# Kernel optimization log

Measured on AMD Instinct MI355X. Metric: run time of the kernel, lower is better.

The kernel has to match this reference:

```python
import jax, jax.numpy as jnp
import numpy as np

B, N, D = 8, 2048, 3
HIDDEN = (64, 128, 256)
LATENT = 128


def _layernorm(x, scale, bias, eps=1e-6):
    mu = jnp.mean(x, axis=-1, keepdims=True)
    var = jnp.mean((x - mu) ** 2, axis=-1, keepdims=True)
    return (x - mu) / jnp.sqrt(var + eps) * scale + bias


def setup_inputs() -> dict:
    key = jax.random.key(0)
    ks = jax.random.split(key, 8)
    inp = {
        "x": jax.random.normal(ks[0], (B, N, D), dtype=jnp.float32),
        "mask": jnp.ones((B, N), dtype=jnp.float32),
    }
    in_d = D
    for i, d in enumerate(HIDDEN):
        inp[f"W{i}"] = (jax.random.normal(ks[1 + i], (in_d, d), dtype=jnp.float32)
                        / np.float32(np.sqrt(in_d)))
        inp[f"b{i}"] = jnp.zeros((d,), dtype=jnp.float32)
        inp[f"g{i}"] = jnp.ones((d,), dtype=jnp.float32)
        inp[f"be{i}"] = jnp.zeros((d,), dtype=jnp.float32)
        in_d = d
    inp["Wz"] = (jax.random.normal(ks[5], (in_d, LATENT), dtype=jnp.float32)
                 / np.float32(np.sqrt(in_d)))
    inp["bz"] = jnp.zeros((LATENT,), dtype=jnp.float32)
    return inp


def reference(x, mask, W0, b0, g0, be0, W1, b1, g1, be1, W2, b2, g2, be2, Wz, bz):
    m = mask[..., None]                                   # (B, N, 1)
    count = jnp.sum(m, axis=1)                            # (B, 1)
    centroid = jnp.sum(x * m, axis=1, keepdims=True) / jnp.maximum(count, 1.0)[:, None, :]
    xc = x - centroid                                     # (B, N, D)

    # Pairwise squared distances; attention depends only on coordinates,
    # so it is identical for every layer -> compute once.
    diff = xc[:, :, None, :] - xc[:, None, :, :]          # (B, N, N, D)
    dist = jnp.sum(diff * diff, axis=-1)                  # (B, N, N)
    attn = jax.nn.softmax(-dist, axis=-1)                 # (B, N, N)

    h = xc
    for W, b, g, be in ((W0, b0, g0, be0), (W1, b1, g1, be1), (W2, b2, g2, be2)):
        h_agg = jnp.einsum('bij,bjd->bid', attn, h)       # weighted aggregation
        h = h_agg @ W + b
        h = _layernorm(h, g, be)
        h = jax.nn.swish(h)

    # Invariant readout: masked mean pool then Dense(latent)
    global_feat = jnp.sum(h * m, axis=1) / jnp.maximum(count, 1.0)
    z = global_feat @ Wz + bz                             # (B, latent)
    return z
```

## Files before the change

### kernel.cpp

```cpp
#include <hip/hip_runtime.h>
#include <hip/hip_bf16.h>

#define BATCH 8
#define NPTS 2048
#define LATENT 128

typedef __attribute__((ext_vector_type(8))) short short8;
typedef __attribute__((ext_vector_type(4))) float f32x4;

__device__ __forceinline__ ushort f2bf(float f) {
  unsigned int b = __float_as_uint(f);
  b += 0x7FFF + ((b >> 16) & 1);
  return (ushort)(b >> 16);
}

typedef unsigned int __attribute__((address_space(1))) gas_uint;
typedef unsigned int __attribute__((address_space(3))) las_uint;
__device__ __forceinline__ void gl_lds16(const void* g, void* l) {
  __builtin_amdgcn_global_load_lds((const gas_uint*)g, (las_uint*)l, 16, 0, 0);
}

#define L2E 1.4426950408889634f
#define SC2 1.6986436f

__device__ __forceinline__ void wtrans_tile(const float* __restrict__ W,
    ushort* __restrict__ WT, int K, int N, int n0, int k0, int tid) {
  __shared__ ushort s[64][72];
  for (int i = tid; i < 64 * 64; i += 256) {
    const int kl = i >> 6, nl = i & 63;
    s[kl][nl] = f2bf(W[(size_t)(k0 + kl) * N + n0 + nl]);
  }
  __syncthreads();
  for (int i = tid; i < 64 * 64; i += 256) {
    const int nl = i >> 6, kl = i & 63;
    WT[(size_t)(n0 + nl) * K + k0 + kl] = s[kl][nl];
  }
}

__global__ __launch_bounds__(256) void setup_kernel(const float* __restrict__ x,
    const float* __restrict__ mask, float4* __restrict__ pnt,
    const float* __restrict__ W1, ushort* __restrict__ WT1,
    const float* __restrict__ W2, ushort* __restrict__ WT2) {
  const int bid = blockIdx.x;
  const int tid = threadIdx.x;
  if (bid >= 8) {
    if (bid < 10) wtrans_tile(W1, WT1, 64, 128, (bid - 8) * 64, 0, tid);
    else {
      const int idx = bid - 10;
      wtrans_tile(W2, WT2, 128, 256, (idx & 3) * 64, (idx >> 2) * 64, tid);
    }
    return;
  }
  const int b = bid;
  const float* xb = x + (size_t)b * NPTS * 3;
  const float* mb = mask + (size_t)b * NPTS;
  float s0 = 0.f, s1 = 0.f, s2 = 0.f, c = 0.f;
  for (int n = tid; n < NPTS; n += 256) {
    float m = mb[n];
    s0 += xb[n * 3 + 0] * m;
    s1 += xb[n * 3 + 1] * m;
    s2 += xb[n * 3 + 2] * m;
    c += m;
  }
  __shared__ float red[4][256];
  red[0][tid] = s0; red[1][tid] = s1; red[2][tid] = s2; red[3][tid] = c;
  __syncthreads();
  for (int off = 128; off > 0; off >>= 1) {
    if (tid < off) {
      red[0][tid] += red[0][tid + off];
      red[1][tid] += red[1][tid + off];
      red[2][tid] += red[2][tid + off];
      red[3][tid] += red[3][tid + off];
    }
    __syncthreads();
  }
  const float cnt = fmaxf(red[3][0], 1.0f);
  const float c0 = red[0][0] / cnt, c1 = red[1][0] / cnt, c2 = red[2][0] / cnt;
  float4* pb = pnt + (size_t)b * NPTS;
  for (int n = tid; n < NPTS; n += 256) {
    const float a0 = xb[n * 3 + 0] - c0;
    const float a1 = xb[n * 3 + 1] - c1;
    const float a2 = xb[n * 3 + 2] - c2;
    pb[n] = make_float4(a0 * SC2, a1 * SC2, a2 * SC2,
                        -(a0 * a0 + a1 * a1 + a2 * a2) * L2E);
  }
}

__global__ __launch_bounds__(512) void layer0_kernel(
    const float4* __restrict__ pnt, const float* __restrict__ W,
    const float* __restrict__ bias, const float* __restrict__ g,
    const float* __restrict__ be, ushort* __restrict__ hout) {
  const int b = blockIdx.y;
  const int i0 = blockIdx.x * 64;
  const int tid = threadIdx.x;
  const int il = tid & 63, part = tid >> 6;
  const float4* pb = pnt + (size_t)b * NPTS;
  const float4 pi = pb[i0 + il];
  float a0 = 0.f, a1 = 0.f, a2 = 0.f, dn = 0.f;
#pragma unroll 8
  for (int j = part * 256; j < part * 256 + 256; j++) {
    const float4 pj = pb[j];
    float arg = pi.w + pj.w;
    arg = fmaf(pi.x, pj.x, arg);
    arg = fmaf(pi.y, pj.y, arg);
    arg = fmaf(pi.z, pj.z, arg);
    const float w = __builtin_amdgcn_exp2f(arg);
    a0 = fmaf(w, pj.x, a0);
    a1 = fmaf(w, pj.y, a1);
    a2 = fmaf(w, pj.z, a2);
    dn += w;
  }
  __shared__ float4 sred[8][64];
  __shared__ float srow[64 * 3];
  __shared__ ushort lt[64][64];
  sred[part][il] = make_float4(a0, a1, a2, dn);
  __syncthreads();
  if (tid < 64) {
    float A0 = 0.f, A1 = 0.f, A2 = 0.f, DN = 0.f;
#pragma unroll
    for (int p = 0; p < 8; p++) {
      const float4 r = sred[p][tid];
      A0 += r.x; A1 += r.y; A2 += r.z; DN += r.w;
    }
    const float inv = 1.0f / (DN * SC2);
    srow[tid * 3 + 0] = A0 * inv;
    srow[tid * 3 + 1] = A1 * inv;
    srow[tid * 3 + 2] = A2 * inv;
  }
  __syncthreads();
  const int wv = tid >> 6, lane = tid & 63;
  const float w0c = W[lane], w1c = W[64 + lane], w2c = W[128 + lane];
  const float gv = g[lane], bev = be[lane], bv = bias[lane];
#pragma unroll
  for (int r = 0; r < 8; r++) {
    const int row = wv * 8 + r;
    float o = bv;
    o = fmaf(srow[row * 3 + 0], w0c, o);
    o = fmaf(srow[row * 3 + 1], w1c, o);
    o = fmaf(srow[row * 3 + 2], w2c, o);
    float m1 = o, m2 = o * o;
#pragma unroll
    for (int off = 32; off > 0; off >>= 1) {
      m1 += __shfl_xor(m1, off, 64);
      m2 += __shfl_xor(m2, off, 64);
    }
    const float mu = m1 / 64.f;
    const float rstd = rsqrtf(m2 / 64.f - mu * mu + 1e-6f);
    const float v = (o - mu) * rstd * gv + bev;
    const float act = v / (1.0f + __expf(-v));
    lt[row][lane] = f2bf(act);
  }
  __syncthreads();
  if (tid < 64) {
    ushort tmp[64];
#pragma unroll
    for (int r = 0; r < 64; r++) tmp[r] = lt[r][tid];
    ushort* dst = hout + ((size_t)b * 64 + tid) * NPTS + i0;
#pragma unroll
    for (int c = 0; c < 8; c++)
      *(uint4*)(dst + c * 8) = *(uint4*)&tmp[c * 8];
  }
}

template <int DIN, int DOUT, bool POOL>
__global__ __launch_bounds__(512, 2) void fused_layer(
    const float4* __restrict__ pnt, const ushort* __restrict__ hT,
    const ushort* __restrict__ WT, const float* __restrict__ bias,
    const float* __restrict__ g, const float* __restrict__ be,
    ushort* __restrict__ hout, const float* __restrict__ mask,
    float* __restrict__ partial) {
  constexpr int NT = DIN / 16;
  constexpr int HALF = NPTS / 2;
  constexpr int TILES = HALF / 64;
  constexpr int NCOL = DOUT / 32;
  constexpr int PS = DIN + 8;
  constexpr int PN = DIN + 4;
  constexpr int SHT_B = 2 * 2 * DIN * 64 * 2;
  constexpr int SPNT_B = 2 * 2 * 64 * 16;
  constexpr int LOOP_B = SHT_B + SPNT_B;
  constexpr int SNUM_B = 64 * PN * 4;
  constexpr int OFF_SROW = SNUM_B;
  constexpr int OFF_SDEN = OFF_SROW + 64 * PS * 2;
  constexpr int OFF_SINV = OFF_SDEN + 256;
  constexpr int OFF_SSTAT = OFF_SINV + 256;
  constexpr int EPI_B = OFF_SSTAT + 1024;
  constexpr int SMEM_B = LOOP_B > EPI_B ? LOOP_B : EPI_B;
  __shared__ __align__(16) char smem[SMEM_B];
  ushort* sht = (ushort*)smem;
  float4* spnt = (float4*)(smem + SHT_B);

  const int b = blockIdx.y;
  const int i0 = blockIdx.x * 64;
  const int tid = threadIdx.x;
  const int wv = tid >> 6, lane = tid & 63;
  const int h = (wv >> 1) & 1;
  const int u = wv & 1;
  const int rg = wv >> 2;
  const int m = lane & 15, q = lane >> 4;
  const float4* pb = pnt + (size_t)b * NPTS;
  const ushort* hb = hT + (size_t)b * DIN * NPTS;

  const float4 pi0 = pb[i0 + rg * 32 + m];
  const float4 pi1 = pb[i0 + rg * 32 + 16 + m];

  f32x4 acc0[NT], acc1[NT];
#pragma unroll
  for (int nt = 0; nt < NT; nt++)
#pragma unroll
    for (int e = 0; e < 4; e++) { acc0[nt][e] = 0.f; acc1[nt][e] = 0.f; }
  float dacc0 = 0.f, dacc1 = 0.f;

  constexpr int NCH = DIN / 32;
  const int srow8 = lane >> 3;
  const int scsrc = (lane & 7) ^ srow8;
  const int jsw = ((lane & 7) << 3) | (lane >> 3);

  auto stage = [&](int t, int bf) {
    const int jb = t * 64;
#pragma unroll
    for (int i = 0; i < NCH; i++) {
      const int idx = wv * NCH + i;
      const int h2 = idx / (DIN / 8);
      const int oct = idx % (DIN / 8);
      const int row = oct * 8 + srow8;
      gl_lds16(hb + (size_t)row * NPTS + h2 * HALF + jb + scsrc * 8,
               sht + ((size_t)(bf * 2 + h2) * DIN + oct * 8) * 64);
    }
    if (wv == 0) {
#pragma unroll
      for (int h2 = 0; h2 < 2; h2++)
        gl_lds16(pb + h2 * HALF + jb + jsw, spnt + (bf * 2 + h2) * 64);
    }
  };

  stage(0, 0);
  __syncthreads();
  for (int t = 0; t < TILES; t++) {
    const int bf = t & 1;
    if (t + 1 < TILES) stage(t + 1, bf ^ 1);
    short8 af0, af1;
#pragma unroll
    for (int jj = 0; jj < 8; jj++) {
      const float4 pj = spnt[(bf * 2 + h) * 64 + ((jj << 3) | (u * 4 + q))];
      float a0 = pi0.w + pj.w;
      a0 = fmaf(pi0.x, pj.x, a0);
      a0 = fmaf(pi0.y, pj.y, a0);
      a0 = fmaf(pi0.z, pj.z, a0);
      float a1 = pi1.w + pj.w;
      a1 = fmaf(pi1.x, pj.x, a1);
      a1 = fmaf(pi1.y, pj.y, a1);
      a1 = fmaf(pi1.z, pj.z, a1);
      const float w0 = __builtin_amdgcn_exp2f(a0);
      const float w1 = __builtin_amdgcn_exp2f(a1);
      dacc0 += w0; dacc1 += w1;
      af0[jj] = (short)f2bf(w0);
      af1[jj] = (short)f2bf(w1);
    }
#pragma unroll
    for (int nt = 0; nt < NT; nt++) {
      const int d = nt * 16 + m;
      const short8 bfr = *(const short8*)
          &sht[((size_t)(bf * 2 + h) * DIN + d) * 64 + (((u * 4 + q) ^ (m & 7)) << 3)];
      acc0[nt] = __builtin_amdgcn_mfma_f32_16x16x32_bf16(af0, bfr, acc0[nt], 0, 0, 0);
      acc1[nt] = __builtin_amdgcn_mfma_f32_16x16x32_bf16(af1, bfr, acc1[nt], 0, 0, 0);
    }
    __syncthreads();
  }

  float* snum = (float*)smem;
  ushort* srow = (ushort*)(smem + OFF_SROW);
  float* sden = (float*)(smem + OFF_SDEN);
  float* sinv = (float*)(smem + OFF_SINV);
  float* sstat = (float*)(smem + OFF_SSTAT);

  dacc0 += __shfl_xor(dacc0, 16, 64);
  dacc0 += __shfl_xor(dacc0, 32, 64);
  dacc1 += __shfl_xor(dacc1, 16, 64);
  dacc1 += __shfl_xor(dacc1, 32, 64);
  const int quarter = wv & 3;
  for (int p = 0; p < 4; p++) {
    if (quarter == p) {
      if (p == 0) {
#pragma unroll
        for (int nt = 0; nt < NT; nt++)
#pragma unroll
          for (int r = 0; r < 4; r++) {
            snum[(rg * 32 + q * 4 + r) * PN + nt * 16 + m] = acc0[nt][r];
            snum[(rg * 32 + 16 + q * 4 + r) * PN + nt * 16 + m] = acc1[nt][r];
          }
        if (q == 0) {
          sden[rg * 32 + m] = dacc0;
          sden[rg * 32 + 16 + m] = dacc1;
        }
      } else {
#pragma unroll
        for (int nt = 0; nt < NT; nt++)
#pragma unroll
          for (int r = 0; r < 4; r++) {
            snum[(rg * 32 + q * 4 + r) * PN + nt * 16 + m] += acc0[nt][r];
            snum[(rg * 32 + 16 + q * 4 + r) * PN + nt * 16 + m] += acc1[nt][r];
          }
        if (q == 0) {
          sden[rg * 32 + m] += dacc0;
          sden[rg * 32 + 16 + m] += dacc1;
        }
      }
    }
    __syncthreads();
  }
  if (tid < 64) sinv[tid] = 1.0f / sden[tid];
  __syncthreads();
  for (int idx = tid; idx < 64 * DIN; idx += 512) {
    const int r = idx / DIN, c = idx & (DIN - 1);
    srow[r * PS + c] = f2bf(snum[r * PN + c] * sinv[r]);
  }
  __syncthreads();

  const int rg2 = wv >> 1, ch = wv & 1;
  short8 afrag[DIN / 32];
#pragma unroll
  for (int kt = 0; kt < DIN / 32; kt++)
    afrag[kt] = *(const short8*)&srow[(rg2 * 16 + m) * PS + kt * 32 + q * 8];
  f32x4 oacc[NCOL];
#pragma unroll
  for (int c = 0; c < NCOL; c++)
#pragma unroll
    for (int e = 0; e < 4; e++) oacc[c][e] = 0.f;
#pragma unroll
  for (int c = 0; c < NCOL; c++) {
    const int n0 = (ch * NCOL + c) * 16;
#pragma unroll
    for (int kt = 0; kt < DIN / 32; kt++) {
      const short8 bfrag = *(const short8*)(WT + (size_t)(n0 + m) * DIN + kt * 32 + q * 8);
      oacc[c] = __builtin_amdgcn_mfma_f32_16x16x32_bf16(afrag[kt], bfrag, oacc[c], 0, 0, 0);
    }
  }

  float bcol[NCOL];
#pragma unroll
  for (int c = 0; c < NCOL; c++) bcol[c] = bias[(ch * NCOL + c) * 16 + m];
#pragma unroll
  for (int r = 0; r < 4; r++) {
    float m1 = 0.f, m2 = 0.f;
#pragma unroll
    for (int c = 0; c < NCOL; c++) {
      const float v = oacc[c][r] + bcol[c];
      m1 += v; m2 += v * v;
    }
#pragma unroll
    for (int off = 8; off > 0; off >>= 1) {
      m1 += __shfl_xor(m1, off, 64);
      m2 += __shfl_xor(m2, off, 64);
    }
    if (m == 0) {
      const int row = rg2 * 16 + q * 4 + r;
      sstat[(row * 2 + ch) * 2 + 0] = m1;
      sstat[(row * 2 + ch) * 2 + 1] = m2;
    }
  }
  __syncthreads();

  ushort* lt = (ushort*)smem;
  float* sp = (float*)smem;
  float pacc[NCOL];
  if (POOL) {
#pragma unroll
    for (int c = 0; c < NCOL; c++) pacc[c] = 0.f;
  }
#pragma unroll
  for (int r = 0; r < 4; r++) {
    const int row = rg2 * 16 + q * 4 + r;
    const float m1 = sstat[(row * 2 + 0) * 2 + 0] + sstat[(row * 2 + 1) * 2 + 0];
    const float m2 = sstat[(row * 2 + 0) * 2 + 1] + sstat[(row * 2 + 1) * 2 + 1];
    const float mu = m1 / DOUT;
    const float rstd = rsqrtf(m2 / DOUT - mu * mu + 1e-6f);
    float mval = 0.f;
    if (POOL) mval = mask[(size_t)b * NPTS + i0 + row];
#pragma unroll
    for (int c = 0; c < NCOL; c++) {
      const int dco = (ch * NCOL + c) * 16 + m;
      const float v = (oacc[c][r] + bcol[c] - mu) * rstd * g[dco] + be[dco];
      const float act = v / (1.0f + __expf(-v));
      if (POOL) pacc[c] = fmaf(act, mval, pacc[c]);
      else lt[row * DOUT + dco] = f2bf(act);
    }
  }
  if (POOL) {
#pragma unroll
    for (int c = 0; c < NCOL; c++) {
      float v = pacc[c];
      v += __shfl_xor(v, 16, 64);
      v += __shfl_xor(v, 32, 64);
      if (q == 0) sp[rg2 * DOUT + (ch * NCOL + c) * 16 + m] = v;
    }
    __syncthreads();
    if (tid < DOUT)
      partial[((size_t)b * (NPTS / 64) + blockIdx.x) * DOUT + tid] =
          (sp[tid] + sp[DOUT + tid]) + (sp[2 * DOUT + tid] + sp[3 * DOUT + tid]);
  } else {
    __syncthreads();
    if (tid < DOUT) {
      ushort tmp[64];
#pragma unroll
      for (int r = 0; r < 64; r++) tmp[r] = lt[r * DOUT + tid];
      ushort* dst = hout + ((size_t)b * DOUT + tid) * NPTS + i0;
#pragma unroll
      for (int c = 0; c < 8; c++)
        *(uint4*)(dst + c * 8) = *(uint4*)&tmp[c * 8];
    }
  }
}

__global__ __launch_bounds__(256) void readout_kernel(
    const float* __restrict__ partial, const float* __restrict__ mask,
    const float* __restrict__ Wz, const float* __restrict__ bz,
    float* __restrict__ out) {
  const int b = blockIdx.x;
  const int tid = threadIdx.x;
  const float* pb = partial + (size_t)b * (NPTS / 64) * 256;
  float s0 = 0.f, s1 = 0.f, s2 = 0.f, s3 = 0.f;
#pragma unroll
  for (int p = 0; p < NPTS / 64; p += 4) {
    s0 += pb[(size_t)(p + 0) * 256 + tid];
    s1 += pb[(size_t)(p + 1) * 256 + tid];
    s2 += pb[(size_t)(p + 2) * 256 + tid];
    s3 += pb[(size_t)(p + 3) * 256 + tid];
  }
  const float s = (s0 + s1) + (s2 + s3);
  const float* mb = mask + (size_t)b * NPTS;
  float c = 0.f;
  for (int n = tid; n < NPTS; n += 256) c += mb[n];
  __shared__ float red[256];
  red[tid] = c;
  __syncthreads();
  for (int off = 128; off > 0; off >>= 1) {
    if (tid < off) red[tid] += red[tid + off];
    __syncthreads();
  }
  const float cnt = fmaxf(red[0], 1.0f);
  __shared__ float gf[256];
  gf[tid] = s / cnt;
  __syncthreads();
  if (tid < LATENT) {
    float z = bz[tid];
#pragma unroll 4
    for (int d = 0; d < 256; d++) z += gf[d] * Wz[(size_t)d * LATENT + tid];
    out[(size_t)b * LATENT + tid] = z;
  }
}

extern "C" void kernel_launch(void* const* d_in, const int* in_sizes, int n_in,
                              void* d_out, int out_size, void* d_ws, size_t ws_size,
                              hipStream_t stream) {
  const float* x    = (const float*)d_in[0];
  const float* mask = (const float*)d_in[1];
  const float* W0   = (const float*)d_in[2];
  const float* b0   = (const float*)d_in[3];
  const float* g0   = (const float*)d_in[4];
  const float* be0  = (const float*)d_in[5];
  const float* W1   = (const float*)d_in[6];
  const float* b1   = (const float*)d_in[7];
  const float* g1   = (const float*)d_in[8];
  const float* be1  = (const float*)d_in[9];
  const float* W2   = (const float*)d_in[10];
  const float* b2   = (const float*)d_in[11];
  const float* g2   = (const float*)d_in[12];
  const float* be2  = (const float*)d_in[13];
  const float* Wz   = (const float*)d_in[14];
  const float* bz   = (const float*)d_in[15];
  float* out = (float*)d_out;

  char* ws = (char*)d_ws;
  float4* pnt     = (float4*)(ws);
  ushort* h1T     = (ushort*)(ws + 262144);
  ushort* h2T     = (ushort*)(ws + 2359296);
  float*  partial = (float*)(ws + 6553600);
  ushort* WT1     = (ushort*)(ws + 6815744);
  ushort* WT2     = (ushort*)(ws + 6832128);

  setup_kernel<<<dim3(18), dim3(256), 0, stream>>>(x, mask, pnt, W1, WT1, W2, WT2);

  layer0_kernel<<<dim3(NPTS / 64, BATCH), dim3(512), 0, stream>>>(
      pnt, W0, b0, g0, be0, h1T);

  fused_layer<64, 128, false><<<dim3(NPTS / 64, BATCH), dim3(512), 0, stream>>>(
      pnt, h1T, WT1, b1, g1, be1, h2T, nullptr, nullptr);

  fused_layer<128, 256, true><<<dim3(NPTS / 64, BATCH), dim3(512), 0, stream>>>(
      pnt, h2T, WT2, b2, g2, be2, nullptr, mask, partial);

  readout_kernel<<<dim3(BATCH), dim3(256), 0, stream>>>(partial, mask, Wz, bz, out);
}
```

Before: 196.8 us.

## Halve fused layer row tile to 32 with 256-thread blocks, bf16 readout weights

The fused attention layers now process 32 query rows per block with 4 waves instead of 64 rows with 8 waves. This doubles the grid to 512 blocks to improve CU fill, at the cost of re-streaming the key/feature tiles twice as often. The weight conversion switches to packed bf16 pair conversion. The readout now reads a pre-transposed bf16 copy of Wz, prepared in setup, and splits the dot product across all 256 threads, which adds a small bf16 rounding error in the final projection.

```diff
diff --git a/kernel.cpp b/kernel.cpp
--- a/kernel.cpp
+++ b/kernel.cpp
@@ -12,6 +12,13 @@
   unsigned int b = __float_as_uint(f);
   b += 0x7FFF + ((b >> 16) & 1);
   return (ushort)(b >> 16);
+}
+__device__ __forceinline__ float bf2f(ushort u) {
+  return __uint_as_float(((unsigned int)u) << 16);
+}
+__device__ __forceinline__ unsigned int pkbf(float a, float b) {
+  __hip_bfloat162 h = __float22bfloat162_rn(make_float2(a, b));
+  return *(unsigned int*)&h;
 }
 
 typedef unsigned int __attribute__((address_space(1))) gas_uint;
@@ -40,14 +47,18 @@
 __global__ __launch_bounds__(256) void setup_kernel(const float* __restrict__ x,
     const float* __restrict__ mask, float4* __restrict__ pnt,
     const float* __restrict__ W1, ushort* __restrict__ WT1,
-    const float* __restrict__ W2, ushort* __restrict__ WT2) {
+    const float* __restrict__ W2, ushort* __restrict__ WT2,
+    const float* __restrict__ Wz, ushort* __restrict__ WzT) {
   const int bid = blockIdx.x;
   const int tid = threadIdx.x;
   if (bid >= 8) {
     if (bid < 10) wtrans_tile(W1, WT1, 64, 128, (bid - 8) * 64, 0, tid);
-    else {
+    else if (bid < 18) {
       const int idx = bid - 10;
       wtrans_tile(W2, WT2, 128, 256, (idx & 3) * 64, (idx >> 2) * 64, tid);
+    } else {
+      const int idx = bid - 18;
+      wtrans_tile(Wz, WzT, 256, 128, (idx & 1) * 64, (idx >> 1) * 64, tid);
     }
     return;
   }
@@ -162,8 +173,8 @@
   }
 }
 
-template <int DIN, int DOUT, bool POOL>
-__global__ __launch_bounds__(512, 2) void fused_layer(
+template <int DIN, int DOUT, bool POOL, int MINW>
+__global__ __launch_bounds__(256, MINW) void fused_layer(
     const float4* __restrict__ pnt, const ushort* __restrict__ hT,
     const ushort* __restrict__ WT, const float* __restrict__ bias,
     const float* __restrict__ g, const float* __restrict__ be,
@@ -178,30 +189,29 @@
   constexpr int SHT_B = 2 * 2 * DIN * 64 * 2;
   constexpr int SPNT_B = 2 * 2 * 64 * 16;
   constexpr int LOOP_B = SHT_B + SPNT_B;
-  constexpr int SNUM_B = 64 * PN * 4;
+  constexpr int SNUM_B = 32 * PN * 4;
   constexpr int OFF_SROW = SNUM_B;
-  constexpr int OFF_SDEN = OFF_SROW + 64 * PS * 2;
-  constexpr int OFF_SINV = OFF_SDEN + 256;
-  constexpr int OFF_SSTAT = OFF_SINV + 256;
-  constexpr int EPI_B = OFF_SSTAT + 1024;
+  constexpr int OFF_SDEN = OFF_SROW + 32 * PS * 2;
+  constexpr int OFF_SINV = OFF_SDEN + 128;
+  constexpr int OFF_SSTAT = OFF_SINV + 128;
+  constexpr int EPI_B = OFF_SSTAT + 512;
   constexpr int SMEM_B = LOOP_B > EPI_B ? LOOP_B : EPI_B;
   __shared__ __align__(16) char smem[SMEM_B];
   ushort* sht = (ushort*)smem;
   float4* spnt = (float4*)(smem + SHT_B);
 
   const int b = blockIdx.y;
-  const int i0 = blockIdx.x * 64;
+  const int i0 = blockIdx.x * 32;
   const int tid = threadIdx.x;
   const int wv = tid >> 6, lane = tid & 63;
-  const int h = (wv >> 1) & 1;
+  const int h = wv >> 1;
   const int u = wv & 1;
-  const int rg = wv >> 2;
   const int m = lane & 15, q = lane >> 4;
   const float4* pb = pnt + (size_t)b * NPTS;
   const ushort* hb = hT + (size_t)b * DIN * NPTS;
 
-  const float4 pi0 = pb[i0 + rg * 32 + m];
-  const float4 pi1 = pb[i0 + rg * 32 + 16 + m];
+  const float4 pi0 = pb[i0 + m];
+  const float4 pi1 = pb[i0 + 16 + m];
 
   f32x4 acc0[NT], acc1[NT];
 #pragma unroll
@@ -210,7 +220,7 @@
     for (int e = 0; e < 4; e++) { acc0[nt][e] = 0.f; acc1[nt][e] = 0.f; }
   float dacc0 = 0.f, dacc1 = 0.f;
 
-  constexpr int NCH = DIN / 32;
+  constexpr int NCH = DIN / 16;
   const int srow8 = lane >> 3;
   const int scsrc = (lane & 7) ^ srow8;
   const int jsw = ((lane & 7) << 3) | (lane >> 3);
@@ -238,7 +248,7 @@
   for (int t = 0; t < TILES; t++) {
     const int bf = t & 1;
     if (t + 1 < TILES) stage(t + 1, bf ^ 1);
-    short8 af0, af1;
+    float w0a[8], w1a[8];
 #pragma unroll
     for (int jj = 0; jj < 8; jj++) {
       const float4 pj = spnt[(bf * 2 + h) * 64 + ((jj << 3) | (u * 4 + q))];
@@ -250,12 +260,18 @@
       a1 = fmaf(pi1.x, pj.x, a1);
       a1 = fmaf(pi1.y, pj.y, a1);
       a1 = fmaf(pi1.z, pj.z, a1);
-      const float w0 = __builtin_amdgcn_exp2f(a0);
-      const float w1 = __builtin_amdgcn_exp2f(a1);
-      dacc0 += w0; dacc1 += w1;
-      af0[jj] = (short)f2bf(w0);
-      af1[jj] = (short)f2bf(w1);
-    }
+      w0a[jj] = __builtin_amdgcn_exp2f(a0);
+      w1a[jj] = __builtin_amdgcn_exp2f(a1);
+      dacc0 += w0a[jj]; dacc1 += w1a[jj];
+    }
+    unsigned int au0[4], au1[4];
+#pragma unroll
+    for (int p = 0; p < 4; p++) {
+      au0[p] = pkbf(w0a[2 * p], w0a[2 * p + 1]);
+      au1[p] = pkbf(w1a[2 * p], w1a[2 * p + 1]);
+    }
+    const short8 af0 = *(short8*)au0;
+    const short8 af1 = *(short8*)au1;
 #pragma unroll
     for (int nt = 0; nt < NT; nt++) {
       const int d = nt * 16 + m;
@@ -277,42 +293,37 @@
   dacc0 += __shfl_xor(dacc0, 32, 64);
   dacc1 += __shfl_xor(dacc1, 16, 64);
   dacc1 += __shfl_xor(dacc1, 32, 64);
-  const int quarter = wv & 3;
   for (int p = 0; p < 4; p++) {
-    if (quarter == p) {
+    if (wv == p) {
       if (p == 0) {
 #pragma unroll
         for (int nt = 0; nt < NT; nt++)
 #pragma unroll
           for (int r = 0; r < 4; r++) {
-            snum[(rg * 32 + q * 4 + r) * PN + nt * 16 + m] = acc0[nt][r];
-            snum[(rg * 32 + 16 + q * 4 + r) * PN + nt * 16 + m] = acc1[nt][r];
+            snum[(q * 4 + r) * PN + nt * 16 + m] = acc0[nt][r];
+            snum[(16 + q * 4 + r) * PN + nt * 16 + m] = acc1[nt][r];
           }
-        if (q == 0) {
-          sden[rg * 32 + m] = dacc0;
-          sden[rg * 32 + 16 + m] = dacc1;
-        }
+        if (q == 0) { sden[m] = dacc0; sden[16 + m] = dacc1; }
       } else {
 #pragma unroll
         for (int nt = 0; nt < NT; nt++)
 #pragma unroll
           for (int r = 0; r < 4; r++) {
-            snum[(rg * 32 + q * 4 + r) * PN + nt * 16 + m] += acc0[nt][r];
-            snum[(rg * 32 + 16 + q * 4 + r) * PN + nt * 16 + m] += acc1[nt][r];
+            snum[(q * 4 + r) * PN + nt * 16 + m] += acc0[nt][r];
+            snum[(16 + q * 4 + r) * PN + nt * 16 + m] += acc1[nt][r];
           }
-        if (q == 0) {
-          sden[rg * 32 + m] += dacc0;
-          sden[rg * 32 + 16 + m] += dacc1;
-        }
+        if (q == 0) { sden[m] += dacc0; sden[16 + m] += dacc1; }
       }
     }
     __syncthreads();
   }
-  if (tid < 64) sinv[tid] = 1.0f / sden[tid];
-  __syncthreads();
-  for (int idx = tid; idx < 64 * DIN; idx += 512) {
-    const int r = idx / DIN, c = idx & (DIN - 1);
-    srow[r * PS + c] = f2bf(snum[r * PN + c] * sinv[r]);
+  if (tid < 32) sinv[tid] = 1.0f / sden[tid];
+  __syncthreads();
+  for (int idx = tid; idx < 32 * (DIN / 2); idx += 256) {
+    const int r = idx / (DIN / 2), c2 = idx % (DIN / 2);
+    const float v0 = snum[r * PN + 2 * c2] * sinv[r];
+    const float v1 = snum[r * PN + 2 * c2 + 1] * sinv[r];
+    *(unsigned int*)&srow[r * PS + 2 * c2] = pkbf(v0, v1);
   }
   __syncthreads();
 
@@ -395,17 +406,17 @@
     }
     __syncthreads();
     if (tid < DOUT)
-      partial[((size_t)b * (NPTS / 64) + blockIdx.x) * DOUT + tid] =
-          (sp[tid] + sp[DOUT + tid]) + (sp[2 * DOUT + tid] + sp[3 * DOUT + tid]);
+      partial[((size_t)b * (NPTS / 32) + blockIdx.x) * DOUT + tid] =
+          sp[tid] + sp[DOUT + tid];
   } else {
     __syncthreads();
     if (tid < DOUT) {
-      ushort tmp[64];
-#pragma unroll
-      for (int r = 0; r < 64; r++) tmp[r] = lt[r * DOUT + tid];
+      ushort tmp[32];
+#pragma unroll
+      for (int r = 0; r < 32; r++) tmp[r] = lt[r * DOUT + tid];
       ushort* dst = hout + ((size_t)b * DOUT + tid) * NPTS + i0;
 #pragma unroll
-      for (int c = 0; c < 8; c++)
+      for (int c = 0; c < 4; c++)
         *(uint4*)(dst + c * 8) = *(uint4*)&tmp[c * 8];
     }
   }
@@ -413,14 +424,14 @@
 
 __global__ __launch_bounds__(256) void readout_kernel(
     const float* __restrict__ partial, const float* __restrict__ mask,
-    const float* __restrict__ Wz, const float* __restrict__ bz,
+    const ushort* __restrict__ WzT, const float* __restrict__ bz,
     float* __restrict__ out) {
   const int b = blockIdx.x;
   const int tid = threadIdx.x;
-  const float* pb = partial + (size_t)b * (NPTS / 64) * 256;
+  const float* pb = partial + (size_t)b * (NPTS / 32) * 256;
   float s0 = 0.f, s1 = 0.f, s2 = 0.f, s3 = 0.f;
-#pragma unroll
-  for (int p = 0; p < NPTS / 64; p += 4) {
+#pragma unroll 4
+  for (int p = 0; p < NPTS / 32; p += 4) {
     s0 += pb[(size_t)(p + 0) * 256 + tid];
     s1 += pb[(size_t)(p + 1) * 256 + tid];
     s2 += pb[(size_t)(p + 2) * 256 + tid];
@@ -441,12 +452,22 @@
   __shared__ float gf[256];
   gf[tid] = s / cnt;
   __syncthreads();
-  if (tid < LATENT) {
-    float z = bz[tid];
+  const int col = tid & 127, part = tid >> 7;
+  float z = 0.f;
+  const ushort* wr = WzT + (size_t)col * 256 + part * 128;
+  const float* gp = gf + part * 128;
 #pragma unroll 4
-    for (int d = 0; d < 256; d++) z += gf[d] * Wz[(size_t)d * LATENT + tid];
-    out[(size_t)b * LATENT + tid] = z;
-  }
+  for (int d = 0; d < 128; d += 8) {
+    const short8 w8 = *(const short8*)(wr + d);
+#pragma unroll
+    for (int e = 0; e < 8; e++)
+      z = fmaf(gp[d + e], bf2f((ushort)w8[e]), z);
+  }
+  __shared__ float zred[256];
+  zred[tid] = z;
+  __syncthreads();
+  if (tid < LATENT)
+    out[(size_t)b * LATENT + tid] = bz[tid] + zred[tid] + zred[128 + tid];
 }
 
 extern "C" void kernel_launch(void* const* d_in, const int* in_sizes, int n_in,
@@ -475,19 +496,21 @@
   ushort* h1T     = (ushort*)(ws + 262144);
   ushort* h2T     = (ushort*)(ws + 2359296);
   float*  partial = (float*)(ws + 6553600);
-  ushort* WT1     = (ushort*)(ws + 6815744);
-  ushort* WT2     = (ushort*)(ws + 6832128);
-
-  setup_kernel<<<dim3(18), dim3(256), 0, stream>>>(x, mask, pnt, W1, WT1, W2, WT2);
+  ushort* WT1     = (ushort*)(ws + 7077888);
+  ushort* WT2     = (ushort*)(ws + 7094272);
+  ushort* WzT     = (ushort*)(ws + 7159808);
+
+  setup_kernel<<<dim3(26), dim3(256), 0, stream>>>(
+      x, mask, pnt, W1, WT1, W2, WT2, Wz, WzT);
 
   layer0_kernel<<<dim3(NPTS / 64, BATCH), dim3(512), 0, stream>>>(
       pnt, W0, b0, g0, be0, h1T);
 
-  fused_layer<64, 128, false><<<dim3(NPTS / 64, BATCH), dim3(512), 0, stream>>>(
+  fused_layer<64, 128, false, 4><<<dim3(NPTS / 32, BATCH), dim3(256), 0, stream>>>(
       pnt, h1T, WT1, b1, g1, be1, h2T, nullptr, nullptr);
 
-  fused_layer<128, 256, true><<<dim3(NPTS / 64, BATCH), dim3(512), 0, stream>>>(
+  fused_layer<128, 256, true, 2><<<dim3(NPTS / 32, BATCH), dim3(256), 0, stream>>>(
       pnt, h2T, WT2, b2, g2, be2, nullptr, mask, partial);
 
-  readout_kernel<<<dim3(BATCH), dim3(256), 0, stream>>>(partial, mask, Wz, bz, out);
-}
+  readout_kernel<<<dim3(BATCH), dim3(256), 0, stream>>>(partial, mask, WzT, bz, out);
+}
```

Result: faster. 175.1 us (-11.0%).
